# Optimization experiments

Hardware: AMD Instinct MI355X
Metric: run time of the kernel (lower is better)

The kernel has to match this reference:

```python
import jax, jax.numpy as jnp
import numpy as np

B, T, H, W, C = 2, 8, 60, 60, 256
HEADS = 8
HD = C // HEADS
WH, WW = 5, 6
SH, SW = 2, 3
N = WH * WW            # 30 tokens per window
NW = (H // WH) * (W // WW)  # 120 windows
HID = 4 * C
SCALE = HD ** -0.5


def _rel_pos_index():
    # standard Swin 2D relative position index, shape (N, N)
    coords = np.stack(np.meshgrid(np.arange(WH), np.arange(WW), indexing='ij')).reshape(2, -1)
    rel = (coords[:, :, None] - coords[:, None, :]).transpose(1, 2, 0).astype(np.int64)
    rel[..., 0] += WH - 1
    rel[..., 1] += WW - 1
    rel[..., 0] *= 2 * WW - 1
    return jnp.asarray(rel.sum(-1))


def _attn_mask():
    # shifted-window attention mask, shape (NW, N, N), values in {0, -100}
    img = np.zeros((H, W))
    cnt = 0
    for hs in (slice(0, -WH), slice(-WH, -SH), slice(-SH, None)):
        for ws in (slice(0, -WW), slice(-WW, -SW), slice(-SW, None)):
            img[hs, ws] = cnt
            cnt += 1
    mw = img.reshape(H // WH, WH, W // WW, WW).transpose(0, 2, 1, 3).reshape(NW, N)
    diff = mw[:, None, :] - mw[:, :, None]
    return jnp.asarray(np.where(diff != 0, -100.0, 0.0).astype(np.float32))


REL_INDEX = _rel_pos_index()
ATTN_MASK = _attn_mask()


def _ln(x, g, b):
    m = x.mean(-1, keepdims=True)
    v = ((x - m) ** 2).mean(-1, keepdims=True)
    return (x - m) / jnp.sqrt(v + 1e-5) * g + b


def setup_inputs() -> dict:
    key = jax.random.key(0)
    ks = jax.random.split(key, 8)
    w_scale = 0.02
    return {
        'x': jax.random.normal(ks[0], (B, T, H, W, C), jnp.float32),
        'contrast_embed': jax.random.normal(ks[1], (B, T, C), jnp.float32),
        'gamma1': jnp.ones((C,), jnp.float32),
        'beta1': jnp.zeros((C,), jnp.float32),
        'Wq': jax.random.normal(ks[2], (C, C), jnp.float32) * w_scale,
        'bq': jnp.zeros((C,), jnp.float32),
        'Wk': jax.random.normal(ks[3], (C, C), jnp.float32) * w_scale,
        'bk': jnp.zeros((C,), jnp.float32),
        'Wv': jax.random.normal(ks[4], (C, C), jnp.float32) * w_scale,
        'bv': jnp.zeros((C,), jnp.float32),
        'rel_bias': jax.random.normal(ks[5], ((2 * WH - 1) * (2 * WW - 1), HEADS), jnp.float32) * w_scale,
        'Wo': jax.random.normal(ks[6], (C, C), jnp.float32) * w_scale,
        'bo': jnp.zeros((C,), jnp.float32),
        'gamma2': jnp.ones((C,), jnp.float32),
        'beta2': jnp.zeros((C,), jnp.float32),
        'W1': jax.random.normal(ks[7], (C, HID), jnp.float32) * w_scale,
        'b1': jnp.zeros((HID,), jnp.float32),
        'W2': jax.random.normal(jax.random.fold_in(key, 99), (HID, C), jnp.float32) * w_scale,
        'b2': jnp.zeros((C,), jnp.float32),
    }


def reference(x, contrast_embed, gamma1, beta1, Wq, bq, Wk, bk, Wv, bv, rel_bias,
              Wo, bo, gamma2, beta2, W1, b1, W2, b2):
    shortcut = x
    xn = _ln(x, gamma1, beta1)
    # cyclic shift (SW-MSA)
    xs = jnp.roll(xn, (-SH, -SW), axis=(2, 3))
    # window partition: (B,T,H,W,C) -> (B*NW, T, N, C)
    w = xs.reshape(B, T, H // WH, WH, W // WW, WW, C)
    w = w.transpose(0, 2, 4, 1, 3, 5, 6).reshape(B * NW, T, N, C)
    # per-contrast positional embedding, broadcast over windows and spatial positions
    pos = jnp.broadcast_to(contrast_embed[:, None, :, None, :], (B, NW, T, 1, C)).reshape(B * NW, T, 1, C)
    wqk = w + pos
    q = (wqk @ Wq + bq).reshape(B * NW, T, N, HEADS, HD)
    k = (wqk @ Wk + bk).reshape(B * NW, T, N, HEADS, HD)
    v = (w @ Wv + bv).reshape(B * NW, T, N, HEADS, HD)
    scores = jnp.einsum('btnhd,btmhd->bthnm', q, k) * SCALE
    bias = rel_bias[REL_INDEX].transpose(2, 0, 1)  # (HEADS, N, N)
    scores = scores + bias
    scores = scores.reshape(B, NW, T, HEADS, N, N) + ATTN_MASK[None, :, None, None]
    attn = jax.nn.softmax(scores, axis=-1).reshape(B * NW, T, HEADS, N, N)
    out = jnp.einsum('bthnm,btmhd->btnhd', attn, v).reshape(B * NW, T, N, C)
    out = out @ Wo + bo
    # window reverse: (B*NW, T, N, C) -> (B, T, H, W, C)
    out = out.reshape(B, H // WH, W // WW, T, WH, WW, C)
    out = out.transpose(0, 3, 1, 4, 2, 5, 6).reshape(B, T, H, W, C)
    out = jnp.roll(out, (SH, SW), axis=(2, 3))
    x1 = shortcut + out
    h = jax.nn.gelu(_ln(x1, gamma2, beta2) @ W1 + b1, approximate=False) @ W2 + b2
    return x1 + h
```

## Files before the change

kernel.cpp:

```cpp
#include <hip/hip_runtime.h>

#define DI __device__ __forceinline__

constexpr int SH_=2, SW_=3;
constexpr int ROWS_=57600;
constexpr float SCALE_=0.17677669529663687f;

typedef unsigned short u16x8 __attribute__((ext_vector_type(8)));
typedef short bf16x8 __attribute__((ext_vector_type(8)));
typedef float f32x4 __attribute__((ext_vector_type(4)));
typedef float f32x16 __attribute__((ext_vector_type(16)));

DI float bf2f(unsigned short u){ return __uint_as_float(((unsigned int)u)<<16); }
DI unsigned short f2bf(float f){
  unsigned int u = __float_as_uint(f);
  u += 0x7fffu + ((u>>16)&1u);
  return (unsigned short)(u>>16);
}
DI float ldf(const void* p, size_t i, int f){
  return f ? ((const float*)p)[i] : bf2f(((const unsigned short*)p)[i]);
}
DI float4 ldf4(const void* p, size_t i, int f){
  if (f) return *((const float4*)((const float*)p + i));
  ushort4 u = *((const ushort4*)((const unsigned short*)p + i));
  return make_float4(bf2f(u.x),bf2f(u.y),bf2f(u.z),bf2f(u.w));
}
DI void stf1(void* p, size_t i, float v, int f){
  if (f) ((float*)p)[i]=v; else ((unsigned short*)p)[i]=f2bf(v);
}

DI void gload16(const void* g, void* l){
  __builtin_amdgcn_global_load_lds((const __attribute__((address_space(1))) unsigned int*)g,
                                   (__attribute__((address_space(3))) unsigned int*)l, 16, 0, 0);
}

DI void xcd_remap(int wg, int nb, int nn, int& mt, int& nt){
  const int q = nb>>3, r = nb&7;
  const int x = wg & 7, i = wg >> 3;
  const int base = (x<r) ? x*(q+1) : r*(q+1) + (x-r)*q;
  const int work = base + i;
  mt = work / nn; nt = work - mt*nn;
}

__global__ void k_detect(const unsigned short* __restrict__ xu, int* __restrict__ flag){
  unsigned short u = xu[threadIdx.x*2];
  int insane = ((u>>7)&0xFF) > 0xC0;
  unsigned long long m = __ballot(insane);
  if (threadIdx.x==0) *flag = m ? 1 : 0;
}

__global__ __launch_bounds__(256) void k_prepw(
    const void* __restrict__ Wq, const void* __restrict__ Wk,
    const void* __restrict__ Wv, const void* __restrict__ Wo,
    const void* __restrict__ W1, const void* __restrict__ W2,
    unsigned short* __restrict__ wt, const int* __restrict__ flagp)
{
  const int f = *flagp;
  const void* src; int kb, total; size_t off;
  switch(blockIdx.y){
    case 0: src=Wq; kb=8;  total=65536;  off=0;      break;
    case 1: src=Wk; kb=8;  total=65536;  off=65536;  break;
    case 2: src=Wv; kb=8;  total=65536;  off=131072; break;
    case 3: src=Wo; kb=8;  total=65536;  off=196608; break;
    case 4: src=W1; kb=8;  total=262144; off=262144; break;
    default:src=W2; kb=10; total=262144; off=524288; break;
  }
  const int i = blockIdx.x*256 + threadIdx.x;
  if (i >= total) return;
  const int K = 1<<kb, N = total>>kb;
  const int n = i>>kb, k = i&(K-1);
  wt[off + (size_t)n*K + k] = f2bf(ldf(src, (size_t)k*N + n, f));
}

__global__ __launch_bounds__(256) void k_posqk(const void* __restrict__ ce,
    const void* __restrict__ Wq, const void* __restrict__ bq,
    const void* __restrict__ Wk, const void* __restrict__ bk,
    float* __restrict__ posq, float* __restrict__ posk, const int* __restrict__ flagp)
{
  const int f = *flagp;
  const int bt = blockIdx.x, co = threadIdx.x;
  float aq = ldf(bq,co,f), ak = ldf(bk,co,f);
  for (int ci=0; ci<256; ++ci){
    float cv = ldf(ce,bt*256+ci,f);
    aq += cv*ldf(Wq,ci*256+co,f);
    ak += cv*ldf(Wk,ci*256+co,f);
  }
  posq[bt*256+co]=aq; posk[bt*256+co]=ak;
}

__global__ __launch_bounds__(256) void k_ln1(const void* __restrict__ x,
    const void* __restrict__ g, const void* __restrict__ be,
    unsigned short* __restrict__ xw, const int* __restrict__ flagp)
{
  const int f = *flagp;
  const int lane = threadIdx.x & 63;
  const int wv   = threadIdx.x >> 6;
  const int rs   = blockIdx.x*4 + wv;
  float4 u = ldf4(x, (size_t)rs*256 + lane*4, f);
  float s = u.x+u.y+u.z+u.w;
  #pragma unroll
  for (int o=32;o;o>>=1) s += __shfl_xor(s,o,64);
  const float mean = s*(1.f/256.f);
  float d0=u.x-mean, d1=u.y-mean, d2=u.z-mean, d3=u.w-mean;
  float qv = d0*d0+d1*d1+d2*d2+d3*d3;
  #pragma unroll
  for (int o=32;o;o>>=1) qv += __shfl_xor(qv,o,64);
  const float rstd = rsqrtf(qv*(1.f/256.f)+1e-5f);
  float4 gu = ldf4(g, lane*4, f);
  float4 bu = ldf4(be, lane*4, f);
  ushort4 o;
  o.x = f2bf(d0*rstd*gu.x+bu.x);
  o.y = f2bf(d1*rstd*gu.y+bu.y);
  o.z = f2bf(d2*rstd*gu.z+bu.z);
  o.w = f2bf(d3*rstd*gu.w+bu.w);
  const int c = rs % 60, r = (rs/60)%60, t = (rs/3600)&7, b = rs/28800;
  int r2 = r - SH_; if (r2<0) r2+=60;
  int c2 = c - SW_; if (c2<0) c2+=60;
  const int a=r2/5, ii=r2%5, bb=c2/6, jj=c2%6;
  const int rw = ((b*120 + a*10+bb)*8 + t)*30 + ii*6+jj;
  *reinterpret_cast<ushort4*>(xw + (size_t)rw*256 + lane*4) = o;
}

__global__ __launch_bounds__(256) void k_ln2(const void* __restrict__ x1,
    const void* __restrict__ g, const void* __restrict__ be,
    unsigned short* __restrict__ xn2, const int* __restrict__ flagp)
{
  const int f = *flagp;
  const int lane = threadIdx.x & 63;
  const int wv   = threadIdx.x >> 6;
  const int rs   = blockIdx.x*4 + wv;
  float4 v = ldf4(x1, (size_t)rs*256 + lane*4, f);
  float s = v.x+v.y+v.z+v.w;
  #pragma unroll
  for (int o=32;o;o>>=1) s += __shfl_xor(s,o,64);
  const float mean = s*(1.f/256.f);
  float d0=v.x-mean, d1=v.y-mean, d2=v.z-mean, d3=v.w-mean;
  float qv = d0*d0+d1*d1+d2*d2+d3*d3;
  #pragma unroll
  for (int o=32;o;o>>=1) qv += __shfl_xor(qv,o,64);
  const float rstd = rsqrtf(qv*(1.f/256.f)+1e-5f);
  float4 gu = ldf4(g, lane*4, f);
  float4 bu = ldf4(be, lane*4, f);
  ushort4 o;
  o.x = f2bf(d0*rstd*gu.x+bu.x);
  o.y = f2bf(d1*rstd*gu.y+bu.y);
  o.z = f2bf(d2*rstd*gu.z+bu.z);
  o.w = f2bf(d3*rstd*gu.w+bu.w);
  *reinterpret_cast<ushort4*>(xn2 + (size_t)rs*256 + lane*4) = o;
}

template<int K>
DI void mfma_core128(const unsigned short* __restrict__ A, const unsigned short* __restrict__ WT,
                     const int m0, const int n0, f32x4 acc[4][2], unsigned short* lds)
{
  constexpr int STEPS = K/32;
  const int tid = threadIdx.x, lane = tid&63, wave = tid>>6;
  const int wm = (wave>>2)*64, wn = (wave&3)*32;
  const int fr = lane&15;
  const int kqs = ((lane>>4) ^ (fr&3))*8;
  #pragma unroll
  for (int i=0;i<4;++i)
    #pragma unroll
    for (int j=0;j<2;++j) acc[i][j] = (f32x4){0.f,0.f,0.f,0.f};
  const int isB = wave>>2;
  const int c0 = (wave&3)*128 + lane;
  const int c1 = c0 + 64;
  const int r0=c0>>2, p0=((c0&3)^(r0&3));
  const int r1=c1>>2, p1=((c1&3)^(r1&3));
  const unsigned short* gb = isB ? (WT + (size_t)n0*K) : (A + (size_t)m0*K);
  const unsigned short* g0 = gb + (size_t)r0*K + p0*8;
  const unsigned short* g1 = gb + (size_t)r1*K + p1*8;
  const int ldso = isB*4096 + (wave&3)*1024;
  #define STAGE_(d,k0) do{ \
    unsigned short* bse = lds + (d)*8192 + ldso; \
    gload16(g0+(k0), bse); \
    gload16(g1+(k0), bse+512); }while(0)
  STAGE_(0,0);
  STAGE_(1,32);
  int cur = 0;
  for (int t=0; t<STEPS; ++t){
    if (t+2 < STEPS){
      int nb = cur+2; if (nb>=3) nb-=3;
      STAGE_(nb, (t+2)*32);
      asm volatile("s_waitcnt vmcnt(4)" ::: "memory");
    } else if (t+2 == STEPS){
      asm volatile("s_waitcnt vmcnt(2)" ::: "memory");
    } else {
      asm volatile("s_waitcnt vmcnt(0)" ::: "memory");
    }
    __builtin_amdgcn_s_barrier();
    const unsigned short* At = lds + cur*8192;
    const unsigned short* Bt = At + 4096;
    bf16x8 af[4], bfv[2];
    #pragma unroll
    for (int mi=0;mi<4;++mi) af[mi]  = *(const bf16x8*)(At + (wm+mi*16+fr)*32 + kqs);
    #pragma unroll
    for (int ni=0;ni<2;++ni) bfv[ni] = *(const bf16x8*)(Bt + (wn+ni*16+fr)*32 + kqs);
    #pragma unroll
    for (int mi=0;mi<4;++mi)
      #pragma unroll
      for (int ni=0;ni<2;++ni)
        acc[mi][ni] = __builtin_amdgcn_mfma_f32_16x16x32_bf16(af[mi], bfv[ni], acc[mi][ni], 0,0,0);
    __builtin_amdgcn_s_barrier();
    cur = (cur+1==3)?0:cur+1;
  }
  #undef STAGE_
}

__global__ __launch_bounds__(512,5) void k_gemm_qkv(const unsigned short* __restrict__ Ain,
    const unsigned short* __restrict__ WT, const float* __restrict__ posq,
    const float* __restrict__ posk, const void* __restrict__ bv,
    unsigned short* __restrict__ qb, unsigned short* __restrict__ kb,
    unsigned short* __restrict__ vb2, const int* __restrict__ flagp)
{
  __shared__ __align__(16) unsigned short lds[24576];
  f32x4 acc[4][2];
  int mt, nt; xcd_remap(blockIdx.x, 2700, 6, mt, nt);
  const int m0 = mt*128, n0g = nt*128;
  mfma_core128<256>(Ain, WT, m0, n0g, acc, lds);
  const int f = *flagp;
  const int lane = threadIdx.x&63, wave = threadIdx.x>>6;
  const int wm = (wave>>2)*64, wn = (wave&3)*32;
  const int fr = lane&15, fq = lane>>4;
  const int seg = nt>>1;
  unsigned short* ob = seg==0? qb : (seg==1? kb : vb2);
  const float* posb = seg==0? posq : posk;
  #pragma unroll
  for (int mi=0;mi<4;++mi){
    #pragma unroll
    for (int r=0;r<4;++r){
      const int row = m0+wm+mi*16+fq*4+r;
      const int bt2 = (row/28800)*8 + (row/30)%8;
      #pragma unroll
      for (int ni=0;ni<2;++ni){
        const int colm = (n0g + wn + ni*16 + fr) & 255;
        const float bvv = (seg<2) ? posb[bt2*256+colm] : ldf(bv,colm,f);
        ob[(size_t)row*256 + colm] = f2bf(acc[mi][ni][r] + bvv);
      }
    }
  }
}

__global__ __launch_bounds__(256) void k_attn(const unsigned short* __restrict__ q,
    const unsigned short* __restrict__ k, const unsigned short* __restrict__ v,
    const void* __restrict__ relb, unsigned short* __restrict__ ao,
    const int* __restrict__ flagp)
{
  __shared__ __align__(16) unsigned short vt[4][32*40];
  __shared__ __align__(16) unsigned short pa[4][32*40];
  const int f = *flagp;
  const int tid = threadIdx.x, lane = tid&63, wave = tid>>6;
  const int task = blockIdx.x*4 + wave;
  const int h = task & 7, bt = task >> 3;
  const int wi = (bt>>3) % 120;
  const int a_ = wi/10, bb_ = wi%10;
  const size_t base = (size_t)bt*7680 + h*32;
  unsigned short* vtw = &vt[wave][0];
  unsigned short* paw = &pa[wave][0];
  if (lane < 60){
    const int m = lane>>1, hf = lane&1;
    const unsigned short* src = v + base + (size_t)m*256 + hf*16;
    u16x8 r0 = *(const u16x8*)(src);
    u16x8 r1 = *(const u16x8*)(src+8);
    #pragma unroll
    for (int j=0;j<8;++j){ vtw[(hf*16+j)*40+m] = r0[j]; vtw[(hf*16+8+j)*40+m] = r1[j]; }
  }
  vtw[(lane>>1)*40 + 30 + (lane&1)] = 0;
  const int n  = lane&31;
  const int hl = lane>>5;
  f32x16 accS = {};
  {
    const unsigned short* ka = k + base + (size_t)n*256 + hl*8;
    const unsigned short* qa = q + base + (size_t)n*256 + hl*8;
    bf16x8 a0 = *(const bf16x8*)(ka);
    bf16x8 b0 = *(const bf16x8*)(qa);
    accS = __builtin_amdgcn_mfma_f32_32x32x16_bf16(a0, b0, accS, 0,0,0);
    bf16x8 a1 = *(const bf16x8*)(ka+16);
    bf16x8 b1 = *(const bf16x8*)(qa+16);
    accS = __builtin_amdgcn_mfma_f32_32x32x16_bf16(a1, b1, accS, 0,0,0);
  }
  const int nc  = (n < 30) ? n : 29;
  const int in_ = nc/6, jn = nc - in_*6;
  const int rn = a_*5+in_, cn = bb_*6+jn;
  const int lnl = (rn<55?0:(rn<58?1:2))*3 + (cn<54?0:(cn<57?1:2));
  #pragma unroll
  for (int r=0;r<16;++r){
    const int m = (r&3) + 8*(r>>2) + 4*hl;
    if (m < 30){
      const int im = m/6, jm = m - im*6;
      const int ridx = (in_-im+4)*11 + (jn-jm+5);
      const float bi = ldf(relb, ridx*8+h, f);
      const int rm = a_*5+im, cm = bb_*6+jm;
      const int lml = (rm<55?0:(rm<58?1:2))*3 + (cm<54?0:(cm<57?1:2));
      accS[r] = accS[r]*SCALE_ + bi + (lnl==lml ? 0.f : -100.f);
    } else accS[r] = -1e30f;
  }
  float mx = accS[0];
  #pragma unroll
  for (int r=1;r<16;++r) mx = fmaxf(mx, accS[r]);
  mx = fmaxf(mx, __shfl_xor(mx, 32, 64));
  float sum = 0.f;
  #pragma unroll
  for (int r=0;r<16;++r){ accS[r] = __expf(accS[r]-mx); sum += accS[r]; }
  sum += __shfl_xor(sum, 32, 64);
  const float inv = 1.f/sum;
  #pragma unroll
  for (int r=0;r<16;++r){
    const int m = (r&3)+8*(r>>2)+4*hl;
    paw[n*40 + m] = f2bf(accS[r]);
  }
  f32x16 accO = {};
  #pragma unroll
  for (int ks=0; ks<2; ++ks){
    bf16x8 av  = *(const bf16x8*)(vtw + n*40 + ks*16 + hl*8);
    bf16x8 pv  = *(const bf16x8*)(paw + n*40 + ks*16 + hl*8);
    accO = __builtin_amdgcn_mfma_f32_32x32x16_bf16(av, pv, accO, 0,0,0);
  }
  if (n < 30){
    #pragma unroll
    for (int g4=0; g4<4; ++g4){
      const int d0 = 8*g4 + 4*hl;
      ushort4 o;
      o.x = f2bf(accO[g4*4+0]*inv);
      o.y = f2bf(accO[g4*4+1]*inv);
      o.z = f2bf(accO[g4*4+2]*inv);
      o.w = f2bf(accO[g4*4+3]*inv);
      *(ushort4*)(ao + base + (size_t)n*256 + d0) = o;
    }
  }
}

__global__ __launch_bounds__(512,5) void k_gemm_wo(const unsigned short* __restrict__ Ain,
    const unsigned short* __restrict__ WT, const void* __restrict__ bias,
    const void* __restrict__ xin, void* __restrict__ x1, const int* __restrict__ flagp)
{
  __shared__ __align__(16) unsigned short lds[24576];
  f32x4 acc[4][2];
  int mt, nt; xcd_remap(blockIdx.x, 900, 2, mt, nt);
  const int m0 = mt*128, n0 = nt*128;
  mfma_core128<256>(Ain, WT, m0, n0, acc, lds);
  const int f = *flagp;
  const int lane = threadIdx.x&63, wave = threadIdx.x>>6;
  const int wm = (wave>>2)*64, wn = (wave&3)*32;
  const int fr = lane&15, fq = lane>>4;
  #pragma unroll
  for (int mi=0;mi<4;++mi){
    #pragma unroll
    for (int r=0;r<4;++r){
      const int rw = m0+wm+mi*16+fq*4+r;
      const int nn = rw%30, t = (rw/30)%8, bw = rw/240;
      const int b = bw/120, wi = bw%120;
      const int a = wi/10, bb2 = wi%10, ii = nn/6, jj = nn%6;
      int rr = a*5+ii+SH_; if (rr>=60) rr-=60;
      int cc = bb2*6+jj+SW_; if (cc>=60) cc-=60;
      const size_t srow = ((size_t)((b*8+t)*60 + rr)*60 + cc);
      #pragma unroll
      for (int ni=0;ni<2;++ni){
        const int col = n0 + wn + ni*16 + fr;
        const float val = ldf(xin, srow*256+col, f) + acc[mi][ni][r] + ldf(bias,col,f);
        stf1(x1, srow*256+col, val, f);
      }
    }
  }
}

__global__ __launch_bounds__(512,5) void k_mlp1(const unsigned short* __restrict__ Ain,
    const unsigned short* __restrict__ WT, const void* __restrict__ bias,
    unsigned short* __restrict__ hb, const int row0, const int* __restrict__ flagp)
{
  __shared__ __align__(16) unsigned short lds[24576];
  f32x4 acc[4][2];
  int mt, nt; xcd_remap(blockIdx.x, 1800, 8, mt, nt);
  const int m0 = row0 + mt*128, n0 = nt*128;
  mfma_core128<256>(Ain, WT, m0, n0, acc, lds);
  const int f = *flagp;
  const int lane = threadIdx.x&63, wave = threadIdx.x>>6;
  const int wm = (wave>>2)*64, wn = (wave&3)*32;
  const int fr = lane&15, fq = lane>>4;
  #pragma unroll
  for (int mi=0;mi<4;++mi){
    #pragma unroll
    for (int ni=0;ni<2;++ni){
      const int col = n0 + wn + ni*16 + fr;
      const float bv = ldf(bias,col,f);
      #pragma unroll
      for (int r=0;r<4;++r){
        const int rl = m0 - row0 + wm + mi*16 + fq*4 + r;
        const float vv = acc[mi][ni][r] + bv;
        const float gg = 0.5f*vv*(1.f+erff(vv*0.70710678118654752f));
        hb[(size_t)rl*1024 + col] = f2bf(gg);
      }
    }
  }
}

__global__ __launch_bounds__(512,5) void k_mlp2(const unsigned short* __restrict__ hbin,
    const unsigned short* __restrict__ WT, const void* __restrict__ bias,
    const void* x1, void* outb, const int row0, const int* __restrict__ flagp)
{
  __shared__ __align__(16) unsigned short lds[24576];
  f32x4 acc[4][2];
  int mt, nt; xcd_remap(blockIdx.x, 450, 2, mt, nt);
  const int m0l = mt*128, n0 = nt*128;
  mfma_core128<1024>(hbin, WT, m0l, n0, acc, lds);
  const int f = *flagp;
  const int lane = threadIdx.x&63, wave = threadIdx.x>>6;
  const int wm = (wave>>2)*64, wn = (wave&3)*32;
  const int fr = lane&15, fq = lane>>4;
  #pragma unroll
  for (int mi=0;mi<4;++mi){
    #pragma unroll
    for (int ni=0;ni<2;++ni){
      const int col = n0 + wn + ni*16 + fr;
      const float bv = ldf(bias,col,f);
      #pragma unroll
      for (int r=0;r<4;++r){
        const int grow = row0 + m0l + wm + mi*16 + fq*4 + r;
        const float val = ldf(x1, (size_t)grow*256+col, f) + acc[mi][ni][r] + bv;
        stf1(outb, (size_t)grow*256+col, val, f);
      }
    }
  }
}

extern "C" void kernel_launch(void* const* d_in, const int* in_sizes, int n_in,
                              void* d_out, int out_size, void* d_ws, size_t ws_size,
                              hipStream_t stream)
{
  const void* x   = d_in[0];
  const void* ce  = d_in[1];
  const void* g1  = d_in[2];
  const void* be1 = d_in[3];
  const void* Wq  = d_in[4];
  const void* bq  = d_in[5];
  const void* Wk  = d_in[6];
  const void* bk  = d_in[7];
  const void* Wv  = d_in[8];
  const void* bv  = d_in[9];
  const void* rb  = d_in[10];
  const void* Wo  = d_in[11];
  const void* bo  = d_in[12];
  const void* g2  = d_in[13];
  const void* be2 = d_in[14];
  const void* W1  = d_in[15];
  const void* b1  = d_in[16];
  const void* W2  = d_in[17];
  const void* b2  = d_in[18];

  char* ws = (char*)d_ws;
  const size_t SZ = (size_t)ROWS_*256*2;
  unsigned short* kbuf = (unsigned short*)(ws);
  unsigned short* vbuf = (unsigned short*)(ws + SZ);
  unsigned short* xw   = (unsigned short*)(ws + 2*SZ);
  unsigned short* qbuf = (unsigned short*)(ws + 3*SZ);
  unsigned short* aob  = xw;
  unsigned short* xn2  = qbuf;
  float* posq = (float*)(ws + 4*SZ);
  float* posk = posq + 16*256;
  int*   flag = (int*)(ws + 4*SZ + 32768);
  unsigned short* wt = (unsigned short*)(ws + 4*SZ + 65536);
  unsigned short* hb = (unsigned short*)ws;
  void* x1 = d_out;

  unsigned short* wtqkv = wt;
  unsigned short* wto = wt + 196608;
  unsigned short* wt1 = wt + 262144;
  unsigned short* wt2 = wt + 524288;

  k_detect<<<1,64,0,stream>>>((const unsigned short*)x, flag);
  k_prepw<<<dim3(1024,6),256,0,stream>>>(Wq,Wk,Wv,Wo,W1,W2, wt, flag);
  k_posqk<<<16,256,0,stream>>>(ce, Wq, bq, Wk, bk, posq, posk, flag);
  k_ln1<<<14400,256,0,stream>>>(x, g1, be1, xw, flag);
  k_gemm_qkv<<<2700,512,0,stream>>>(xw, wtqkv, posq, posk, bv, qbuf, kbuf, vbuf, flag);
  k_attn<<<3840,256,0,stream>>>(qbuf, kbuf, vbuf, rb, aob, flag);
  k_gemm_wo<<<900,512,0,stream>>>(aob, wto, bo, x, x1, flag);
  k_ln2<<<14400,256,0,stream>>>(x1, g2, be2, xn2, flag);
  for (int chk=0; chk<2; ++chk){
    const int row0 = chk*28800;
    k_mlp1<<<1800,512,0,stream>>>(xn2, wt1, b1, hb, row0, flag);
    k_mlp2<<<450,512,0,stream>>>(hb, wt2, b2, x1, d_out, row0, flag);
  }
}
```

Before: 338.3 us.

## Stage GEMM epilogues through LDS for coalesced stores; keep x1 in bf16 workspace

All four GEMM epilogues (qkv, wo, mlp1, mlp2) now write their bias-added results into a padded LDS tile and then issue 16-byte vectorized, row-contiguous global stores, replacing scattered 2-byte per-lane stores. The residual x1 is kept as a bf16 workspace buffer instead of being written to the output, which halves its traffic when inputs are fp32. Buffers are reassigned so that hb, xn2 and x1b do not alias. In exchange there is an extra LDS round trip and barrier per tile, and rounding x1 (and the GEMM output before the residual add) to bf16 changes numerics when running in fp32.

```diff
diff --git a/kernel.cpp b/kernel.cpp
--- a/kernel.cpp
+++ b/kernel.cpp
@@ -24,9 +24,6 @@
   if (f) return *((const float4*)((const float*)p + i));
   ushort4 u = *((const ushort4*)((const unsigned short*)p + i));
   return make_float4(bf2f(u.x),bf2f(u.y),bf2f(u.z),bf2f(u.w));
-}
-DI void stf1(void* p, size_t i, float v, int f){
-  if (f) ((float*)p)[i]=v; else ((unsigned short*)p)[i]=f2bf(v);
 }
 
 DI void gload16(const void* g, void* l){
@@ -121,7 +118,7 @@
   *reinterpret_cast<ushort4*>(xw + (size_t)rw*256 + lane*4) = o;
 }
 
-__global__ __launch_bounds__(256) void k_ln2(const void* __restrict__ x1,
+__global__ __launch_bounds__(256) void k_ln2(const unsigned short* __restrict__ x1b,
     const void* __restrict__ g, const void* __restrict__ be,
     unsigned short* __restrict__ xn2, const int* __restrict__ flagp)
 {
@@ -129,7 +126,7 @@
   const int lane = threadIdx.x & 63;
   const int wv   = threadIdx.x >> 6;
   const int rs   = blockIdx.x*4 + wv;
-  float4 v = ldf4(x1, (size_t)rs*256 + lane*4, f);
+  float4 v = ldf4(x1b, (size_t)rs*256 + lane*4, 0);
   float s = v.x+v.y+v.z+v.w;
   #pragma unroll
   for (int o=32;o;o>>=1) s += __shfl_xor(s,o,64);
@@ -216,10 +213,10 @@
   __shared__ __align__(16) unsigned short lds[24576];
   f32x4 acc[4][2];
   int mt, nt; xcd_remap(blockIdx.x, 2700, 6, mt, nt);
-  const int m0 = mt*128, n0g = nt*128;
-  mfma_core128<256>(Ain, WT, m0, n0g, acc, lds);
-  const int f = *flagp;
-  const int lane = threadIdx.x&63, wave = threadIdx.x>>6;
+  const int m0 = mt*128;
+  mfma_core128<256>(Ain, WT, m0, nt*128, acc, lds);
+  const int f = *flagp;
+  const int tid = threadIdx.x, lane = tid&63, wave = tid>>6;
   const int wm = (wave>>2)*64, wn = (wave&3)*32;
   const int fr = lane&15, fq = lane>>4;
   const int seg = nt>>1;
@@ -229,15 +226,25 @@
   for (int mi=0;mi<4;++mi){
     #pragma unroll
     for (int r=0;r<4;++r){
-      const int row = m0+wm+mi*16+fq*4+r;
-      const int bt2 = (row/28800)*8 + (row/30)%8;
+      const int row = wm+mi*16+fq*4+r;
+      const int grow = m0+row;
+      const int bt2 = (grow/28800)*8 + (grow/30)%8;
       #pragma unroll
       for (int ni=0;ni<2;++ni){
-        const int colm = (n0g + wn + ni*16 + fr) & 255;
+        const int lcol = wn+ni*16+fr;
+        const int colm = (nt&1)*128 + lcol;
         const float bvv = (seg<2) ? posb[bt2*256+colm] : ldf(bv,colm,f);
-        ob[(size_t)row*256 + colm] = f2bf(acc[mi][ni][r] + bvv);
+        lds[row*132+lcol] = f2bf(acc[mi][ni][r] + bvv);
       }
     }
+  }
+  __syncthreads();
+  const int row = tid>>2;
+  unsigned short* dst = ob + (size_t)(m0+row)*256 + (nt&1)*128;
+  #pragma unroll
+  for (int j=0;j<4;++j){
+    const int ci = j*4 + (tid&3);
+    *(u16x8*)(dst + ci*8) = *(const u16x8*)(lds + row*132 + ci*8);
   }
 }
 
@@ -332,7 +339,8 @@
 
 __global__ __launch_bounds__(512,5) void k_gemm_wo(const unsigned short* __restrict__ Ain,
     const unsigned short* __restrict__ WT, const void* __restrict__ bias,
-    const void* __restrict__ xin, void* __restrict__ x1, const int* __restrict__ flagp)
+    const void* __restrict__ xin, unsigned short* __restrict__ x1b,
+    const int* __restrict__ flagp)
 {
   __shared__ __align__(16) unsigned short lds[24576];
   f32x4 acc[4][2];
@@ -340,27 +348,44 @@
   const int m0 = mt*128, n0 = nt*128;
   mfma_core128<256>(Ain, WT, m0, n0, acc, lds);
   const int f = *flagp;
-  const int lane = threadIdx.x&63, wave = threadIdx.x>>6;
+  const int tid = threadIdx.x, lane = tid&63, wave = tid>>6;
   const int wm = (wave>>2)*64, wn = (wave&3)*32;
   const int fr = lane&15, fq = lane>>4;
   #pragma unroll
   for (int mi=0;mi<4;++mi){
     #pragma unroll
-    for (int r=0;r<4;++r){
-      const int rw = m0+wm+mi*16+fq*4+r;
-      const int nn = rw%30, t = (rw/30)%8, bw = rw/240;
-      const int b = bw/120, wi = bw%120;
-      const int a = wi/10, bb2 = wi%10, ii = nn/6, jj = nn%6;
-      int rr = a*5+ii+SH_; if (rr>=60) rr-=60;
-      int cc = bb2*6+jj+SW_; if (cc>=60) cc-=60;
-      const size_t srow = ((size_t)((b*8+t)*60 + rr)*60 + cc);
+    for (int ni=0;ni<2;++ni){
+      const int lcol = wn+ni*16+fr;
+      const float bvv = ldf(bias, n0+lcol, f);
       #pragma unroll
-      for (int ni=0;ni<2;++ni){
-        const int col = n0 + wn + ni*16 + fr;
-        const float val = ldf(xin, srow*256+col, f) + acc[mi][ni][r] + ldf(bias,col,f);
-        stf1(x1, srow*256+col, val, f);
+      for (int r=0;r<4;++r){
+        const int row = wm+mi*16+fq*4+r;
+        lds[row*132+lcol] = f2bf(acc[mi][ni][r] + bvv);
       }
     }
+  }
+  __syncthreads();
+  const int row = tid>>2;
+  const int rw = m0+row;
+  const int nn = rw%30, t = (rw/30)%8, bw = rw/240;
+  const int b = bw/120, wi = bw%120;
+  const int a = wi/10, bb2 = wi%10, ii = nn/6, jj = nn%6;
+  int rr = a*5+ii+SH_; if (rr>=60) rr-=60;
+  int cc = bb2*6+jj+SW_; if (cc>=60) cc-=60;
+  const size_t srow = ((size_t)((b*8+t)*60 + rr)*60 + cc);
+  #pragma unroll
+  for (int j=0;j<4;++j){
+    const int ci = j*4 + (tid&3);
+    const int col = n0 + ci*8;
+    u16x8 vv = *(const u16x8*)(lds + row*132 + ci*8);
+    float4 xa = ldf4(xin, srow*256+col,   f);
+    float4 xbv= ldf4(xin, srow*256+col+4, f);
+    u16x8 o;
+    o[0]=f2bf(bf2f(vv[0])+xa.x); o[1]=f2bf(bf2f(vv[1])+xa.y);
+    o[2]=f2bf(bf2f(vv[2])+xa.z); o[3]=f2bf(bf2f(vv[3])+xa.w);
+    o[4]=f2bf(bf2f(vv[4])+xbv.x); o[5]=f2bf(bf2f(vv[5])+xbv.y);
+    o[6]=f2bf(bf2f(vv[6])+xbv.z); o[7]=f2bf(bf2f(vv[7])+xbv.w);
+    *(u16x8*)(x1b + srow*256 + col) = o;
   }
 }
 
@@ -374,29 +399,37 @@
   const int m0 = row0 + mt*128, n0 = nt*128;
   mfma_core128<256>(Ain, WT, m0, n0, acc, lds);
   const int f = *flagp;
-  const int lane = threadIdx.x&63, wave = threadIdx.x>>6;
+  const int tid = threadIdx.x, lane = tid&63, wave = tid>>6;
   const int wm = (wave>>2)*64, wn = (wave&3)*32;
   const int fr = lane&15, fq = lane>>4;
   #pragma unroll
   for (int mi=0;mi<4;++mi){
     #pragma unroll
     for (int ni=0;ni<2;++ni){
-      const int col = n0 + wn + ni*16 + fr;
-      const float bv = ldf(bias,col,f);
+      const int lcol = wn+ni*16+fr;
+      const float bvv = ldf(bias, n0+lcol, f);
       #pragma unroll
       for (int r=0;r<4;++r){
-        const int rl = m0 - row0 + wm + mi*16 + fq*4 + r;
-        const float vv = acc[mi][ni][r] + bv;
-        const float gg = 0.5f*vv*(1.f+erff(vv*0.70710678118654752f));
-        hb[(size_t)rl*1024 + col] = f2bf(gg);
+        const int row = wm+mi*16+fq*4+r;
+        const float vv = acc[mi][ni][r] + bvv;
+        lds[row*132+lcol] = f2bf(0.5f*vv*(1.f+erff(vv*0.70710678118654752f)));
       }
     }
+  }
+  __syncthreads();
+  const int row = tid>>2;
+  unsigned short* dst = hb + (size_t)(mt*128+row)*1024 + n0;
+  #pragma unroll
+  for (int j=0;j<4;++j){
+    const int ci = j*4 + (tid&3);
+    *(u16x8*)(dst + ci*8) = *(const u16x8*)(lds + row*132 + ci*8);
   }
 }
 
 __global__ __launch_bounds__(512,5) void k_mlp2(const unsigned short* __restrict__ hbin,
     const unsigned short* __restrict__ WT, const void* __restrict__ bias,
-    const void* x1, void* outb, const int row0, const int* __restrict__ flagp)
+    const unsigned short* __restrict__ x1b, void* __restrict__ outb,
+    const int row0, const int* __restrict__ flagp)
 {
   __shared__ __align__(16) unsigned short lds[24576];
   f32x4 acc[4][2];
@@ -404,21 +437,44 @@
   const int m0l = mt*128, n0 = nt*128;
   mfma_core128<1024>(hbin, WT, m0l, n0, acc, lds);
   const int f = *flagp;
-  const int lane = threadIdx.x&63, wave = threadIdx.x>>6;
+  const int tid = threadIdx.x, lane = tid&63, wave = tid>>6;
   const int wm = (wave>>2)*64, wn = (wave&3)*32;
   const int fr = lane&15, fq = lane>>4;
   #pragma unroll
   for (int mi=0;mi<4;++mi){
     #pragma unroll
     for (int ni=0;ni<2;++ni){
-      const int col = n0 + wn + ni*16 + fr;
-      const float bv = ldf(bias,col,f);
+      const int lcol = wn+ni*16+fr;
+      const float bvv = ldf(bias, n0+lcol, f);
       #pragma unroll
       for (int r=0;r<4;++r){
-        const int grow = row0 + m0l + wm + mi*16 + fq*4 + r;
-        const float val = ldf(x1, (size_t)grow*256+col, f) + acc[mi][ni][r] + bv;
-        stf1(outb, (size_t)grow*256+col, val, f);
+        const int row = wm+mi*16+fq*4+r;
+        lds[row*132+lcol] = f2bf(acc[mi][ni][r] + bvv);
       }
+    }
+  }
+  __syncthreads();
+  const int row = tid>>2;
+  const size_t grow = (size_t)(row0 + m0l + row);
+  #pragma unroll
+  for (int j=0;j<4;++j){
+    const int ci = j*4 + (tid&3);
+    const int col = n0 + ci*8;
+    u16x8 vv = *(const u16x8*)(lds + row*132 + ci*8);
+    u16x8 xv = *(const u16x8*)(x1b + grow*256 + col);
+    if (f){
+      float4 o0, o1;
+      o0.x=bf2f(vv[0])+bf2f(xv[0]); o0.y=bf2f(vv[1])+bf2f(xv[1]);
+      o0.z=bf2f(vv[2])+bf2f(xv[2]); o0.w=bf2f(vv[3])+bf2f(xv[3]);
+      o1.x=bf2f(vv[4])+bf2f(xv[4]); o1.y=bf2f(vv[5])+bf2f(xv[5]);
+      o1.z=bf2f(vv[6])+bf2f(xv[6]); o1.w=bf2f(vv[7])+bf2f(xv[7]);
+      *(float4*)((float*)outb + grow*256 + col)     = o0;
+      *(float4*)((float*)outb + grow*256 + col + 4) = o1;
+    } else {
+      u16x8 o;
+      #pragma unroll
+      for (int e=0;e<8;++e) o[e] = f2bf(bf2f(vv[e])+bf2f(xv[e]));
+      *(u16x8*)((unsigned short*)outb + grow*256 + col) = o;
     }
   }
 }
@@ -454,13 +510,13 @@
   unsigned short* xw   = (unsigned short*)(ws + 2*SZ);
   unsigned short* qbuf = (unsigned short*)(ws + 3*SZ);
   unsigned short* aob  = xw;
-  unsigned short* xn2  = qbuf;
+  unsigned short* xn2  = kbuf;
+  unsigned short* x1b  = qbuf;
+  unsigned short* hb   = vbuf;
   float* posq = (float*)(ws + 4*SZ);
   float* posk = posq + 16*256;
   int*   flag = (int*)(ws + 4*SZ + 32768);
   unsigned short* wt = (unsigned short*)(ws + 4*SZ + 65536);
-  unsigned short* hb = (unsigned short*)ws;
-  void* x1 = d_out;
 
   unsigned short* wtqkv = wt;
   unsigned short* wto = wt + 196608;
@@ -473,11 +529,11 @@
   k_ln1<<<14400,256,0,stream>>>(x, g1, be1, xw, flag);
   k_gemm_qkv<<<2700,512,0,stream>>>(xw, wtqkv, posq, posk, bv, qbuf, kbuf, vbuf, flag);
   k_attn<<<3840,256,0,stream>>>(qbuf, kbuf, vbuf, rb, aob, flag);
-  k_gemm_wo<<<900,512,0,stream>>>(aob, wto, bo, x, x1, flag);
-  k_ln2<<<14400,256,0,stream>>>(x1, g2, be2, xn2, flag);
+  k_gemm_wo<<<900,512,0,stream>>>(aob, wto, bo, x, x1b, flag);
+  k_ln2<<<14400,256,0,stream>>>(x1b, g2, be2, xn2, flag);
   for (int chk=0; chk<2; ++chk){
     const int row0 = chk*28800;
     k_mlp1<<<1800,512,0,stream>>>(xn2, wt1, b1, hb, row0, flag);
-    k_mlp2<<<450,512,0,stream>>>(hb, wt2, b2, x1, d_out, row0, flag);
-  }
-}
+    k_mlp2<<<450,512,0,stream>>>(hb, wt2, b2, x1b, d_out, row0, flag);
+  }
+}
```

Result: faster. 305.9 us (-9.6%).
